# Kernel tuning notes

Hardware: AMD Instinct MI355X
Metric: run time of the kernel (lower is better)

Reference implementation:

```python
import jax, jax.numpy as jnp
import numpy as np

N_NODES = 100000


def gcn_conv(x, src, dst, W, b, n_nodes):
    """PyG GCNConv: add self-loops, symmetric deg^-1/2 normalization,
    linear transform, scatter-add aggregation, bias."""
    loop = jnp.arange(n_nodes, dtype=src.dtype)
    s = jnp.concatenate([src, loop])
    d = jnp.concatenate([dst, loop])
    # degree of destination nodes (includes self-loops)
    deg = jax.ops.segment_sum(jnp.ones(s.shape[0], dtype=x.dtype), d,
                              num_segments=n_nodes)
    dis = jnp.where(deg > 0, jax.lax.rsqrt(deg), 0.0)  # deg^-1/2
    norm = dis[s] * dis[d]                              # [E+N]
    h = x @ W                                           # [N, out]
    msg = h[s] * norm[:, None]                          # gather + scale
    out = jax.ops.segment_sum(msg, d, num_segments=n_nodes)  # scatter-add
    return out + b


def setup_inputs() -> dict:
    key = jax.random.key(0)
    k1, k2, k3, k4 = jax.random.split(key, 4)
    F_in, H, C = 500, 64, 10
    x = jax.random.normal(k1, (N_NODES, F_in), dtype=jnp.float32)
    edge_index = jax.random.randint(k2, (2, 1600000), 0, N_NODES,
                                    dtype=jnp.int32)
    W1 = jax.random.normal(k3, (F_in, H), dtype=jnp.float32) / np.sqrt(F_in)
    b1 = jnp.zeros((H,), dtype=jnp.float32)
    W2 = jax.random.normal(k4, (H, C), dtype=jnp.float32) / np.sqrt(H)
    b2 = jnp.zeros((C,), dtype=jnp.float32)
    return {"x": x, "edge_index": edge_index,
            "W1": W1, "b1": b1, "W2": W2, "b2": b2}


def reference(x, edge_index, W1, b1, W2, b2):
    src, dst = edge_index[0], edge_index[1]
    h = gcn_conv(x, src, dst, W1, b1, N_NODES)
    h = jax.nn.relu(h)
    # dropout is identity at inference (training=False)
    out = gcn_conv(h, src, dst, W2, b2, N_NODES)
    return out
```

## Files before the change

kernel.cpp:

```cpp
#include <hip/hip_runtime.h>

#define F_IN 500
#define HDIM 64
#define CDIM 10
#define KPAD 512
#define NSTAGE 16

typedef __attribute__((ext_vector_type(8))) short bf16x8;
typedef __attribute__((ext_vector_type(4))) float floatx4;

__device__ inline unsigned short f2bf(float f) {
    unsigned int u = __float_as_uint(f);
    u += 0x7fffu + ((u >> 16) & 1u);
    return (unsigned short)(u >> 16);
}

__global__ void deg_count_kernel(const int* __restrict__ dst, int E,
                                 int* __restrict__ deg) {
    int e = blockIdx.x * blockDim.x + threadIdx.x;
    if (e < E) atomicAdd(&deg[dst[e]], 1);
}

__global__ void scan_block_kernel(const int* __restrict__ deg,
                                  int* __restrict__ row_ptr,
                                  int* __restrict__ blk_sum,
                                  float* __restrict__ dis, int Np1) {
    __shared__ int wsum[16];
    int i = blockIdx.x * 1024 + threadIdx.x;
    int v = (i < Np1 - 1) ? deg[i] : 0;
    if (i < Np1 - 1) dis[i] = rsqrtf((float)(v + 1));
    int lane = threadIdx.x & 63;
    int wid = threadIdx.x >> 6;
    int x = v;
#pragma unroll
    for (int off = 1; off < 64; off <<= 1) {
        int y = __shfl_up(x, off);
        if (lane >= off) x += y;
    }
    if (lane == 63) wsum[wid] = x;
    __syncthreads();
    if (threadIdx.x < 16) {
        int ws = wsum[threadIdx.x];
#pragma unroll
        for (int off = 1; off < 16; off <<= 1) {
            int y = __shfl_up(ws, off);
            if ((int)threadIdx.x >= off) ws += y;
        }
        wsum[threadIdx.x] = ws;
    }
    __syncthreads();
    int wp = (wid > 0) ? wsum[wid - 1] : 0;
    if (i < Np1) row_ptr[i] = wp + x - v;
    if (threadIdx.x == 1023) blk_sum[blockIdx.x] = wp + x;
}

__global__ void scan_top_kernel(int* __restrict__ blk_sum, int nb) {
    int carry = 0;
    for (int base = 0; base < nb; base += 64) {
        int i = base + (int)threadIdx.x;
        int v = (i < nb) ? blk_sum[i] : 0;
        int x = v;
#pragma unroll
        for (int off = 1; off < 64; off <<= 1) {
            int y = __shfl_up(x, off);
            if ((int)threadIdx.x >= off) x += y;
        }
        if (i < nb) blk_sum[i] = carry + x - v;
        carry += __shfl(x, 63);
    }
}

__global__ void scan_add_kernel(int* __restrict__ row_ptr,
                                const int* __restrict__ blk_sum, int Np1) {
    int i = blockIdx.x * blockDim.x + threadIdx.x;
    if (i < Np1) row_ptr[i] += blk_sum[i >> 10];
}

__global__ void csr_fill_kernel(const int* __restrict__ src,
                                const int* __restrict__ dst,
                                const int* __restrict__ row_ptr,
                                int* __restrict__ cursor,
                                int* __restrict__ csr_src, int E) {
    int e = blockIdx.x * blockDim.x + threadIdx.x;
    if (e >= E) return;
    int d = dst[e];
    int pos = atomicAdd(&cursor[d], 1);
    csr_src[row_ptr[d] + pos] = src[e];
}

__global__ void wprep_kernel(const float* __restrict__ W1,
                             unsigned short* __restrict__ whf,
                             unsigned short* __restrict__ wlf) {
    int idx = blockIdx.x * 256 + threadIdx.x;
    if (idx >= KPAD * HDIM) return;
    int k = idx >> 6;
    int f = idx & 63;
    float w = (k < F_IN) ? W1[k * HDIM + f] : 0.f;
    unsigned int b = __float_as_uint(w);
    unsigned short hh = (unsigned short)(b >> 16);
    float wl = w - __uint_as_float(b & 0xffff0000u);
    unsigned short ll = (unsigned short)(__float_as_uint(wl) >> 16);
    int kb = k >> 5, q = (k >> 3) & 3, j = k & 7;
    int fb = f >> 4, fl = f & 15;
    int lane = (q << 4) | fl;
    size_t o = ((((size_t)kb * 4 + fb) * 64 + lane) << 3) | (size_t)j;
    whf[o] = hh;
    wlf[o] = ll;
}

__global__ __launch_bounds__(256) void gemm1_kernel(
        const float* __restrict__ x,
        const unsigned short* __restrict__ whf,
        const unsigned short* __restrict__ wlf,
        const float* __restrict__ dis,
        unsigned short* __restrict__ h1b, int N) {
    const int lane = threadIdx.x & 63;
    const int wid = (blockIdx.x * 256 + threadIdx.x) >> 6;
    const int n0 = wid * 32;
    if (n0 >= N) return;
    const int q = lane >> 4;
    const int fl = lane & 15;

    int r0 = n0 + fl;       if (r0 >= N) r0 = N - 1;
    int r1 = n0 + 16 + fl;  if (r1 >= N) r1 = N - 1;
    const float* xp0 = x + (size_t)r0 * F_IN + q * 8;
    const float* xp1 = x + (size_t)r1 * F_IN + q * 8;

    floatx4 acc[2][4];
#pragma unroll
    for (int t = 0; t < 2; ++t)
#pragma unroll
        for (int fb = 0; fb < 4; ++fb) acc[t][fb] = (floatx4){0.f, 0.f, 0.f, 0.f};

    const bf16x8* whv = (const bf16x8*)whf;
    const bf16x8* wlv = (const bf16x8*)wlf;

    for (int kb = 0; kb < NSTAGE; ++kb) {
        float xv0[8], xv1[8];
        if (kb < NSTAGE - 1) {
            float4 a = *(const float4*)(xp0 + kb * 32);
            float4 b = *(const float4*)(xp0 + kb * 32 + 4);
            xv0[0] = a.x; xv0[1] = a.y; xv0[2] = a.z; xv0[3] = a.w;
            xv0[4] = b.x; xv0[5] = b.y; xv0[6] = b.z; xv0[7] = b.w;
            float4 c = *(const float4*)(xp1 + kb * 32);
            float4 d = *(const float4*)(xp1 + kb * 32 + 4);
            xv1[0] = c.x; xv1[1] = c.y; xv1[2] = c.z; xv1[3] = c.w;
            xv1[4] = d.x; xv1[5] = d.y; xv1[6] = d.z; xv1[7] = d.w;
        } else {
#pragma unroll
            for (int j = 0; j < 8; ++j) {
                int kk = kb * 32 + q * 8 + j;
                xv0[j] = (kk < F_IN) ? xp0[kb * 32 + j] : 0.f;
                xv1[j] = (kk < F_IN) ? xp1[kb * 32 + j] : 0.f;
            }
        }
        bf16x8 xh0, xl0, xh1, xl1;
#pragma unroll
        for (int j = 0; j < 8; ++j) {
            unsigned int b0 = __float_as_uint(xv0[j]);
            xh0[j] = (short)(b0 >> 16);
            float res0 = xv0[j] - __uint_as_float(b0 & 0xffff0000u);
            xl0[j] = (short)(__float_as_uint(res0) >> 16);
            unsigned int b1 = __float_as_uint(xv1[j]);
            xh1[j] = (short)(b1 >> 16);
            float res1 = xv1[j] - __uint_as_float(b1 & 0xffff0000u);
            xl1[j] = (short)(__float_as_uint(res1) >> 16);
        }
#pragma unroll
        for (int fb = 0; fb < 4; ++fb) {
            bf16x8 bh = whv[(size_t)(kb * 4 + fb) * 64 + lane];
            bf16x8 bl = wlv[(size_t)(kb * 4 + fb) * 64 + lane];
            acc[0][fb] = __builtin_amdgcn_mfma_f32_16x16x32_bf16(xh0, bh, acc[0][fb], 0, 0, 0);
            acc[0][fb] = __builtin_amdgcn_mfma_f32_16x16x32_bf16(xl0, bh, acc[0][fb], 0, 0, 0);
            acc[0][fb] = __builtin_amdgcn_mfma_f32_16x16x32_bf16(xh0, bl, acc[0][fb], 0, 0, 0);
            acc[1][fb] = __builtin_amdgcn_mfma_f32_16x16x32_bf16(xh1, bh, acc[1][fb], 0, 0, 0);
            acc[1][fb] = __builtin_amdgcn_mfma_f32_16x16x32_bf16(xl1, bh, acc[1][fb], 0, 0, 0);
            acc[1][fb] = __builtin_amdgcn_mfma_f32_16x16x32_bf16(xh1, bl, acc[1][fb], 0, 0, 0);
        }
    }
#pragma unroll
    for (int t = 0; t < 2; ++t) {
#pragma unroll
        for (int r = 0; r < 4; ++r) {
            int node = n0 + t * 16 + q * 4 + r;
            if (node < N) {
                float dn = dis[node];
#pragma unroll
                for (int fb = 0; fb < 4; ++fb) {
                    h1b[(size_t)node * HDIM + fb * 16 + fl] =
                        f2bf(acc[t][fb][r] * dn);
                }
            }
        }
    }
}

__global__ void gather1_kernel(const int* __restrict__ row_ptr,
                               const int* __restrict__ csr_src,
                               const float* __restrict__ dis,
                               const unsigned short* __restrict__ h1b,
                               float* __restrict__ agg1, int N) {
    int nid = blockIdx.x * 4 + (threadIdx.x >> 6);
    if (nid >= N) return;
    int node = __builtin_amdgcn_readfirstlane(nid);
    int lane = threadIdx.x & 63;
    int half = lane >> 5;
    int c = lane & 31;
    int beg = row_ptr[node];
    int end = row_ptr[node + 1];
    float dd = dis[node];
    float a0 = 0.f, a1 = 0.f;
    if (half == 0) {
        unsigned int w = *reinterpret_cast<const unsigned int*>(
            h1b + (size_t)node * HDIM + 2 * c);
        a0 = __uint_as_float(w << 16);
        a1 = __uint_as_float(w & 0xffff0000u);
    }
    int p = beg + half;
    for (; p + 6 < end; p += 8) {
        int s0 = csr_src[p];
        int s1 = csr_src[p + 2];
        int s2 = csr_src[p + 4];
        int s3 = csr_src[p + 6];
        unsigned int w0 = *reinterpret_cast<const unsigned int*>(h1b + (size_t)s0 * HDIM + 2 * c);
        unsigned int w1 = *reinterpret_cast<const unsigned int*>(h1b + (size_t)s1 * HDIM + 2 * c);
        unsigned int w2 = *reinterpret_cast<const unsigned int*>(h1b + (size_t)s2 * HDIM + 2 * c);
        unsigned int w3 = *reinterpret_cast<const unsigned int*>(h1b + (size_t)s3 * HDIM + 2 * c);
        a0 += __uint_as_float(w0 << 16);
        a1 += __uint_as_float(w0 & 0xffff0000u);
        a0 += __uint_as_float(w1 << 16);
        a1 += __uint_as_float(w1 & 0xffff0000u);
        a0 += __uint_as_float(w2 << 16);
        a1 += __uint_as_float(w2 & 0xffff0000u);
        a0 += __uint_as_float(w3 << 16);
        a1 += __uint_as_float(w3 & 0xffff0000u);
    }
    for (; p < end; p += 2) {
        int s0 = csr_src[p];
        unsigned int w0 = *reinterpret_cast<const unsigned int*>(h1b + (size_t)s0 * HDIM + 2 * c);
        a0 += __uint_as_float(w0 << 16);
        a1 += __uint_as_float(w0 & 0xffff0000u);
    }
    a0 += __shfl_xor(a0, 32);
    a1 += __shfl_xor(a1, 32);
    if (half == 0) {
        *reinterpret_cast<float2*>(agg1 + (size_t)node * HDIM + 2 * c) =
            make_float2(a0 * dd, a1 * dd);
    }
}

__global__ void layer2_kernel(const float* __restrict__ agg1,
                              const float* __restrict__ b1,
                              const float* __restrict__ W2,
                              const float* __restrict__ dis,
                              float* __restrict__ h2s, int N) {
    int n = blockIdx.x * blockDim.x + threadIdx.x;
    if (n >= N) return;
    const float* ar = agg1 + (size_t)n * HDIM;
    float t[HDIM];
#pragma unroll
    for (int c = 0; c < HDIM; ++c) {
        float v = ar[c] + b1[c];
        t[c] = v > 0.f ? v : 0.f;
    }
    float dn = dis[n];
    float* h2r = h2s + (size_t)n * CDIM;
#pragma unroll
    for (int j = 0; j < CDIM; ++j) {
        float acc = 0.f;
#pragma unroll
        for (int c = 0; c < HDIM; ++c) acc = fmaf(t[c], W2[c * CDIM + j], acc);
        h2r[j] = acc * dn;
    }
}

__global__ void gather2_kernel(const int* __restrict__ row_ptr,
                               const int* __restrict__ csr_src,
                               const float* __restrict__ dis,
                               const float* __restrict__ h2s,
                               const float* __restrict__ b2,
                               float* __restrict__ out, int N) {
    int nid = blockIdx.x * 4 + (threadIdx.x >> 6);
    if (nid >= N) return;
    int node = __builtin_amdgcn_readfirstlane(nid);
    int lane = threadIdx.x & 63;
    int g = lane >> 4;
    int j = lane & 15;
    int jj = (j < CDIM) ? j : CDIM - 1;
    int beg = row_ptr[node];
    int end = row_ptr[node + 1];
    float acc = 0.f;
    for (int p = beg + g; p < end; p += 4) {
        int s = csr_src[p];
        acc += h2s[(size_t)s * CDIM + jj];
    }
    acc += __shfl_xor(acc, 16);
    acc += __shfl_xor(acc, 32);
    if (lane < CDIM) {
        float dd = dis[node];
        out[(size_t)node * CDIM + lane] =
            b2[lane] + dd * (acc + h2s[(size_t)node * CDIM + lane]);
    }
}

static inline char* align256(char* p) {
    return (char*)(((uintptr_t)p + 255) & ~(uintptr_t)255);
}

extern "C" void kernel_launch(void* const* d_in, const int* in_sizes, int n_in,
                              void* d_out, int out_size, void* d_ws,
                              size_t ws_size, hipStream_t stream) {
    const float* x  = (const float*)d_in[0];
    const int*   ei = (const int*)d_in[1];
    const float* W1 = (const float*)d_in[2];
    const float* b1 = (const float*)d_in[3];
    const float* W2 = (const float*)d_in[4];
    const float* b2 = (const float*)d_in[5];

    const int N = in_sizes[0] / F_IN;
    const int E = in_sizes[1] / 2;
    const int* src = ei;
    const int* dst = ei + E;
    float* out = (float*)d_out;

    const int Np1 = N + 1;
    const int nscan_blocks = (Np1 + 1023) / 1024;

    char* w = (char*)d_ws;
    int* deg = (int*)w;                  w = align256(w + (size_t)N * 4);
    int* cursor = (int*)w;               w = align256(w + (size_t)N * 4);
    float* dis = (float*)w;              w = align256(w + (size_t)N * 4);
    int* row_ptr = (int*)w;              w = align256(w + (size_t)(N + 4) * 4);
    int* blk_sum = (int*)w;              w = align256(w + (size_t)nscan_blocks * 4);
    int* csr_src = (int*)w;              w = align256(w + (size_t)E * 4);
    unsigned short* whf = (unsigned short*)w;  w = align256(w + (size_t)KPAD * HDIM * 2);
    unsigned short* wlf = (unsigned short*)w;  w = align256(w + (size_t)KPAD * HDIM * 2);
    unsigned short* h1b = (unsigned short*)w;  w = align256(w + (size_t)N * HDIM * 2);
    float* agg1 = (float*)w;             w = align256(w + (size_t)N * HDIM * 4);
    float* h2s = (float*)h1b;

    hipMemsetAsync(deg, 0, (size_t)N * 2 * 4, stream);
    hipMemsetAsync(cursor, 0, (size_t)N * 4, stream);

    wprep_kernel<<<(KPAD * HDIM + 255) / 256, 256, 0, stream>>>(W1, whf, wlf);
    deg_count_kernel<<<(E + 255) / 256, 256, 0, stream>>>(dst, E, deg);
    scan_block_kernel<<<nscan_blocks, 1024, 0, stream>>>(deg, row_ptr, blk_sum,
                                                         dis, Np1);
    scan_top_kernel<<<1, 64, 0, stream>>>(blk_sum, nscan_blocks);
    scan_add_kernel<<<(Np1 + 255) / 256, 256, 0, stream>>>(row_ptr, blk_sum,
                                                           Np1);
    csr_fill_kernel<<<(E + 255) / 256, 256, 0, stream>>>(src, dst, row_ptr,
                                                         cursor, csr_src, E);
    {
        int nwaves = (N + 31) / 32;
        int blocks = (nwaves + 3) / 4;
        gemm1_kernel<<<blocks, 256, 0, stream>>>(x, whf, wlf, dis, h1b, N);
    }
    gather1_kernel<<<(N + 3) / 4, 256, 0, stream>>>(row_ptr, csr_src, dis, h1b,
                                                    agg1, N);
    layer2_kernel<<<(N + 255) / 256, 256, 0, stream>>>(agg1, b1, W2, dis, h2s,
                                                       N);
    gather2_kernel<<<(N + 3) / 4, 256, 0, stream>>>(row_ptr, csr_src, dis, h2s,
                                                    b2, out, N);
}
```

Baseline: 587.4 us.

## Fuse layer-1 gather with bias/ReLU/W2 projection and drop scan-add pass

The first-layer gather now also applies bias, ReLU and the 64x10 W2 projection in-register using cross-lane shuffle reductions, which removes the agg1 intermediate and the separate layer2 kernel. The scan_add kernel is eliminated by adding the block offset (blk_sum) wherever row_ptr is read. The two memsets are merged into one. Gather kernels switch to persistent grid-stride loops with 16 lanes per edge group. h2s is padded to a 16-float stride. The cost is extra shuffles per node in the fused kernel and an extra blk_sum load at every row_ptr access.

```diff
diff --git a/kernel.cpp b/kernel.cpp
--- a/kernel.cpp
+++ b/kernel.cpp
@@ -5,6 +5,7 @@
 #define CDIM 10
 #define KPAD 512
 #define NSTAGE 16
+#define H2LD 16
 
 typedef __attribute__((ext_vector_type(8))) short bf16x8;
 typedef __attribute__((ext_vector_type(4))) float floatx4;
@@ -14,6 +15,8 @@
     u += 0x7fffu + ((u >> 16) & 1u);
     return (unsigned short)(u >> 16);
 }
+__device__ inline float bflo(unsigned int u) { return __uint_as_float(u << 16); }
+__device__ inline float bfhi(unsigned int u) { return __uint_as_float(u & 0xffff0000u); }
 
 __global__ void deg_count_kernel(const int* __restrict__ dst, int E,
                                  int* __restrict__ deg) {
@@ -70,22 +73,17 @@
     }
 }
 
-__global__ void scan_add_kernel(int* __restrict__ row_ptr,
-                                const int* __restrict__ blk_sum, int Np1) {
-    int i = blockIdx.x * blockDim.x + threadIdx.x;
-    if (i < Np1) row_ptr[i] += blk_sum[i >> 10];
-}
-
 __global__ void csr_fill_kernel(const int* __restrict__ src,
                                 const int* __restrict__ dst,
                                 const int* __restrict__ row_ptr,
+                                const int* __restrict__ blk_sum,
                                 int* __restrict__ cursor,
                                 int* __restrict__ csr_src, int E) {
     int e = blockIdx.x * blockDim.x + threadIdx.x;
     if (e >= E) return;
     int d = dst[e];
     int pos = atomicAdd(&cursor[d], 1);
-    csr_src[row_ptr[d] + pos] = src[e];
+    csr_src[row_ptr[d] + blk_sum[d >> 10] + pos] = src[e];
 }
 
 __global__ void wprep_kernel(const float* __restrict__ W1,
@@ -195,111 +193,116 @@
     }
 }
 
-__global__ void gather1_kernel(const int* __restrict__ row_ptr,
-                               const int* __restrict__ csr_src,
-                               const float* __restrict__ dis,
-                               const unsigned short* __restrict__ h1b,
-                               float* __restrict__ agg1, int N) {
-    int nid = blockIdx.x * 4 + (threadIdx.x >> 6);
-    if (nid >= N) return;
-    int node = __builtin_amdgcn_readfirstlane(nid);
-    int lane = threadIdx.x & 63;
-    int half = lane >> 5;
-    int c = lane & 31;
-    int beg = row_ptr[node];
-    int end = row_ptr[node + 1];
-    float dd = dis[node];
-    float a0 = 0.f, a1 = 0.f;
-    if (half == 0) {
-        unsigned int w = *reinterpret_cast<const unsigned int*>(
-            h1b + (size_t)node * HDIM + 2 * c);
-        a0 = __uint_as_float(w << 16);
-        a1 = __uint_as_float(w & 0xffff0000u);
-    }
-    int p = beg + half;
-    for (; p + 6 < end; p += 8) {
-        int s0 = csr_src[p];
-        int s1 = csr_src[p + 2];
-        int s2 = csr_src[p + 4];
-        int s3 = csr_src[p + 6];
-        unsigned int w0 = *reinterpret_cast<const unsigned int*>(h1b + (size_t)s0 * HDIM + 2 * c);
-        unsigned int w1 = *reinterpret_cast<const unsigned int*>(h1b + (size_t)s1 * HDIM + 2 * c);
-        unsigned int w2 = *reinterpret_cast<const unsigned int*>(h1b + (size_t)s2 * HDIM + 2 * c);
-        unsigned int w3 = *reinterpret_cast<const unsigned int*>(h1b + (size_t)s3 * HDIM + 2 * c);
-        a0 += __uint_as_float(w0 << 16);
-        a1 += __uint_as_float(w0 & 0xffff0000u);
-        a0 += __uint_as_float(w1 << 16);
-        a1 += __uint_as_float(w1 & 0xffff0000u);
-        a0 += __uint_as_float(w2 << 16);
-        a1 += __uint_as_float(w2 & 0xffff0000u);
-        a0 += __uint_as_float(w3 << 16);
-        a1 += __uint_as_float(w3 & 0xffff0000u);
-    }
-    for (; p < end; p += 2) {
-        int s0 = csr_src[p];
-        unsigned int w0 = *reinterpret_cast<const unsigned int*>(h1b + (size_t)s0 * HDIM + 2 * c);
-        a0 += __uint_as_float(w0 << 16);
-        a1 += __uint_as_float(w0 & 0xffff0000u);
-    }
-    a0 += __shfl_xor(a0, 32);
-    a1 += __shfl_xor(a1, 32);
-    if (half == 0) {
-        *reinterpret_cast<float2*>(agg1 + (size_t)node * HDIM + 2 * c) =
-            make_float2(a0 * dd, a1 * dd);
-    }
-}
-
-__global__ void layer2_kernel(const float* __restrict__ agg1,
-                              const float* __restrict__ b1,
-                              const float* __restrict__ W2,
-                              const float* __restrict__ dis,
-                              float* __restrict__ h2s, int N) {
-    int n = blockIdx.x * blockDim.x + threadIdx.x;
-    if (n >= N) return;
-    const float* ar = agg1 + (size_t)n * HDIM;
-    float t[HDIM];
-#pragma unroll
-    for (int c = 0; c < HDIM; ++c) {
-        float v = ar[c] + b1[c];
-        t[c] = v > 0.f ? v : 0.f;
-    }
-    float dn = dis[n];
-    float* h2r = h2s + (size_t)n * CDIM;
-#pragma unroll
-    for (int j = 0; j < CDIM; ++j) {
+__global__ __launch_bounds__(256) void gather1_mlp_kernel(
+        const int* __restrict__ row_ptr, const int* __restrict__ blk_sum,
+        const int* __restrict__ csr_src, const float* __restrict__ dis,
+        const unsigned short* __restrict__ h1b,
+        const float* __restrict__ b1, const float* __restrict__ W2,
+        float* __restrict__ h2s, int N) {
+    const int lane = threadIdx.x & 63;
+    const int g = lane >> 4;
+    const int c = lane & 15;
+    const int gw = (blockIdx.x * 256 + threadIdx.x) >> 6;
+    const int nwaves = (gridDim.x * 256) >> 6;
+
+    float w2r[4][CDIM];
+#pragma unroll
+    for (int i = 0; i < 4; ++i)
+#pragma unroll
+        for (int j = 0; j < CDIM; ++j) w2r[i][j] = W2[(4 * c + i) * CDIM + j];
+    float4 b1q = *(const float4*)(b1 + 4 * c);
+    float b1r[4] = {b1q.x, b1q.y, b1q.z, b1q.w};
+
+    for (int nid = gw; nid < N; nid += nwaves) {
+        int node = __builtin_amdgcn_readfirstlane(nid);
+        int beg = row_ptr[node] + blk_sum[node >> 10];
+        int end = row_ptr[node + 1] + blk_sum[(node + 1) >> 10];
+        float dd = dis[node];
+        float a0 = 0.f, a1 = 0.f, a2 = 0.f, a3 = 0.f;
+        if (g == 0) {
+            uint2 w = *(const uint2*)(h1b + (size_t)node * HDIM + 4 * c);
+            a0 = bflo(w.x); a1 = bfhi(w.x); a2 = bflo(w.y); a3 = bfhi(w.y);
+        }
+        int p = beg + g;
+        for (; p + 12 < end; p += 16) {
+            int s0 = csr_src[p];
+            int s1 = csr_src[p + 4];
+            int s2 = csr_src[p + 8];
+            int s3 = csr_src[p + 12];
+            uint2 w0 = *(const uint2*)(h1b + (size_t)s0 * HDIM + 4 * c);
+            uint2 w1 = *(const uint2*)(h1b + (size_t)s1 * HDIM + 4 * c);
+            uint2 w2 = *(const uint2*)(h1b + (size_t)s2 * HDIM + 4 * c);
+            uint2 w3 = *(const uint2*)(h1b + (size_t)s3 * HDIM + 4 * c);
+            a0 += bflo(w0.x); a1 += bfhi(w0.x); a2 += bflo(w0.y); a3 += bfhi(w0.y);
+            a0 += bflo(w1.x); a1 += bfhi(w1.x); a2 += bflo(w1.y); a3 += bfhi(w1.y);
+            a0 += bflo(w2.x); a1 += bfhi(w2.x); a2 += bflo(w2.y); a3 += bfhi(w2.y);
+            a0 += bflo(w3.x); a1 += bfhi(w3.x); a2 += bflo(w3.y); a3 += bfhi(w3.y);
+        }
+        for (; p < end; p += 4) {
+            int s0 = csr_src[p];
+            uint2 w0 = *(const uint2*)(h1b + (size_t)s0 * HDIM + 4 * c);
+            a0 += bflo(w0.x); a1 += bfhi(w0.x); a2 += bflo(w0.y); a3 += bfhi(w0.y);
+        }
+        a0 += __shfl_xor(a0, 16); a0 += __shfl_xor(a0, 32);
+        a1 += __shfl_xor(a1, 16); a1 += __shfl_xor(a1, 32);
+        a2 += __shfl_xor(a2, 16); a2 += __shfl_xor(a2, 32);
+        a3 += __shfl_xor(a3, 16); a3 += __shfl_xor(a3, 32);
+        float t0 = fmaf(a0, dd, b1r[0]); t0 = t0 > 0.f ? t0 : 0.f;
+        float t1 = fmaf(a1, dd, b1r[1]); t1 = t1 > 0.f ? t1 : 0.f;
+        float t2 = fmaf(a2, dd, b1r[2]); t2 = t2 > 0.f ? t2 : 0.f;
+        float t3 = fmaf(a3, dd, b1r[3]); t3 = t3 > 0.f ? t3 : 0.f;
+        float pj[CDIM];
+#pragma unroll
+        for (int j = 0; j < CDIM; ++j)
+            pj[j] = fmaf(t0, w2r[0][j],
+                    fmaf(t1, w2r[1][j],
+                    fmaf(t2, w2r[2][j], t3 * w2r[3][j])));
+#pragma unroll
+        for (int off = 1; off < 16; off <<= 1)
+#pragma unroll
+            for (int j = 0; j < CDIM; ++j) pj[j] += __shfl_xor(pj[j], off);
+        float v = pj[0];
+#pragma unroll
+        for (int j = 1; j < CDIM; ++j) v = (lane == j) ? pj[j] : v;
+        if (lane < CDIM) h2s[(size_t)node * H2LD + lane] = v * dd;
+    }
+}
+
+__global__ __launch_bounds__(256) void gather2_kernel(
+        const int* __restrict__ row_ptr, const int* __restrict__ blk_sum,
+        const int* __restrict__ csr_src, const float* __restrict__ dis,
+        const float* __restrict__ h2s, const float* __restrict__ b2,
+        float* __restrict__ out, int N) {
+    const int lane = threadIdx.x & 63;
+    const int g = lane >> 4;
+    const int j = lane & 15;
+    const int gw = (blockIdx.x * 256 + threadIdx.x) >> 6;
+    const int nwaves = (gridDim.x * 256) >> 6;
+
+    for (int nid = gw; nid < N; nid += nwaves) {
+        int node = __builtin_amdgcn_readfirstlane(nid);
+        int beg = row_ptr[node] + blk_sum[node >> 10];
+        int end = row_ptr[node + 1] + blk_sum[(node + 1) >> 10];
         float acc = 0.f;
-#pragma unroll
-        for (int c = 0; c < HDIM; ++c) acc = fmaf(t[c], W2[c * CDIM + j], acc);
-        h2r[j] = acc * dn;
-    }
-}
-
-__global__ void gather2_kernel(const int* __restrict__ row_ptr,
-                               const int* __restrict__ csr_src,
-                               const float* __restrict__ dis,
-                               const float* __restrict__ h2s,
-                               const float* __restrict__ b2,
-                               float* __restrict__ out, int N) {
-    int nid = blockIdx.x * 4 + (threadIdx.x >> 6);
-    if (nid >= N) return;
-    int node = __builtin_amdgcn_readfirstlane(nid);
-    int lane = threadIdx.x & 63;
-    int g = lane >> 4;
-    int j = lane & 15;
-    int jj = (j < CDIM) ? j : CDIM - 1;
-    int beg = row_ptr[node];
-    int end = row_ptr[node + 1];
-    float acc = 0.f;
-    for (int p = beg + g; p < end; p += 4) {
-        int s = csr_src[p];
-        acc += h2s[(size_t)s * CDIM + jj];
-    }
-    acc += __shfl_xor(acc, 16);
-    acc += __shfl_xor(acc, 32);
-    if (lane < CDIM) {
-        float dd = dis[node];
-        out[(size_t)node * CDIM + lane] =
-            b2[lane] + dd * (acc + h2s[(size_t)node * CDIM + lane]);
+        int p = beg + g;
+        for (; p + 4 < end; p += 8) {
+            int s0 = csr_src[p];
+            int s1 = csr_src[p + 4];
+            float v0 = (j < CDIM) ? h2s[(size_t)s0 * H2LD + j] : 0.f;
+            float v1 = (j < CDIM) ? h2s[(size_t)s1 * H2LD + j] : 0.f;
+            acc += v0 + v1;
+        }
+        for (; p < end; p += 4) {
+            int s0 = csr_src[p];
+            acc += (j < CDIM) ? h2s[(size_t)s0 * H2LD + j] : 0.f;
+        }
+        acc += __shfl_xor(acc, 16);
+        acc += __shfl_xor(acc, 32);
+        if (lane < CDIM) {
+            float dd = dis[node];
+            out[(size_t)node * CDIM + lane] =
+                b2[lane] + dd * (acc + h2s[(size_t)node * H2LD + lane]);
+        }
     }
 }
 
@@ -329,6 +332,7 @@
     char* w = (char*)d_ws;
     int* deg = (int*)w;                  w = align256(w + (size_t)N * 4);
     int* cursor = (int*)w;               w = align256(w + (size_t)N * 4);
+    char* zero_end = w;
     float* dis = (float*)w;              w = align256(w + (size_t)N * 4);
     int* row_ptr = (int*)w;              w = align256(w + (size_t)(N + 4) * 4);
     int* blk_sum = (int*)w;              w = align256(w + (size_t)nscan_blocks * 4);
@@ -336,30 +340,25 @@
     unsigned short* whf = (unsigned short*)w;  w = align256(w + (size_t)KPAD * HDIM * 2);
     unsigned short* wlf = (unsigned short*)w;  w = align256(w + (size_t)KPAD * HDIM * 2);
     unsigned short* h1b = (unsigned short*)w;  w = align256(w + (size_t)N * HDIM * 2);
-    float* agg1 = (float*)w;             w = align256(w + (size_t)N * HDIM * 4);
-    float* h2s = (float*)h1b;
-
-    hipMemsetAsync(deg, 0, (size_t)N * 2 * 4, stream);
-    hipMemsetAsync(cursor, 0, (size_t)N * 4, stream);
+    float* h2s = (float*)w;              w = align256(w + (size_t)N * H2LD * 4);
+
+    hipMemsetAsync(deg, 0, (size_t)(zero_end - (char*)deg), stream);
 
     wprep_kernel<<<(KPAD * HDIM + 255) / 256, 256, 0, stream>>>(W1, whf, wlf);
     deg_count_kernel<<<(E + 255) / 256, 256, 0, stream>>>(dst, E, deg);
     scan_block_kernel<<<nscan_blocks, 1024, 0, stream>>>(deg, row_ptr, blk_sum,
                                                          dis, Np1);
     scan_top_kernel<<<1, 64, 0, stream>>>(blk_sum, nscan_blocks);
-    scan_add_kernel<<<(Np1 + 255) / 256, 256, 0, stream>>>(row_ptr, blk_sum,
-                                                           Np1);
     csr_fill_kernel<<<(E + 255) / 256, 256, 0, stream>>>(src, dst, row_ptr,
-                                                         cursor, csr_src, E);
+                                                         blk_sum, cursor,
+                                                         csr_src, E);
     {
         int nwaves = (N + 31) / 32;
         int blocks = (nwaves + 3) / 4;
         gemm1_kernel<<<blocks, 256, 0, stream>>>(x, whf, wlf, dis, h1b, N);
     }
-    gather1_kernel<<<(N + 3) / 4, 256, 0, stream>>>(row_ptr, csr_src, dis, h1b,
-                                                    agg1, N);
-    layer2_kernel<<<(N + 255) / 256, 256, 0, stream>>>(agg1, b1, W2, dis, h2s,
-                                                       N);
-    gather2_kernel<<<(N + 3) / 4, 256, 0, stream>>>(row_ptr, csr_src, dis, h2s,
-                                                    b2, out, N);
-}
+    gather1_mlp_kernel<<<2048, 256, 0, stream>>>(row_ptr, blk_sum, csr_src,
+                                                 dis, h1b, b1, W2, h2s, N);
+    gather2_kernel<<<2048, 256, 0, stream>>>(row_ptr, blk_sum, csr_src, dis,
+                                             h2s, b2, out, N);
+}
```

After: 595.8 us. No clear change (+1.4%).
